# Optimization experiments

Hardware: AMD Instinct MI355X
Metric: run time of the kernel (lower is better)

## Reference

```python
import jax, jax.numpy as jnp
import numpy as np

V_WORD, V_CHAR = 50000, 128
EMB, CEMB, FILT, K = 300, 32, 4, 3
HID = 512
T, B, W = 128, 64, 16
OUT = 20
CCH = CEMB * FILT  # 128 conv output channels
LSTM_IN = EMB + CCH  # 428


def setup_inputs() -> dict:
    key = jax.random.key(0)
    ks = jax.random.split(key, 20)
    s = 0.1  # matches init_weights std
    inp = {
        "words": jax.random.randint(ks[0], (T, B), 0, V_WORD),
        "chars": jax.random.randint(ks[1], (B, T, W), 0, V_CHAR),
        "emb_W": s * jax.random.normal(ks[2], (V_WORD, EMB), jnp.float32),
        "char_emb_W": s * jax.random.normal(ks[3], (V_CHAR, CEMB), jnp.float32),
        "conv_W": s * jax.random.normal(ks[4], (CCH, 1, K), jnp.float32),
        "conv_b": s * jax.random.normal(ks[5], (CCH,), jnp.float32),
        "Wih_f": s * jax.random.normal(ks[6], (4 * HID, LSTM_IN), jnp.float32),
        "Whh_f": s * jax.random.normal(ks[7], (4 * HID, HID), jnp.float32),
        "bih_f": s * jax.random.normal(ks[8], (4 * HID,), jnp.float32),
        "bhh_f": s * jax.random.normal(ks[9], (4 * HID,), jnp.float32),
        "Wih_b": s * jax.random.normal(ks[10], (4 * HID, LSTM_IN), jnp.float32),
        "Whh_b": s * jax.random.normal(ks[11], (4 * HID, HID), jnp.float32),
        "bih_b": s * jax.random.normal(ks[12], (4 * HID,), jnp.float32),
        "bhh_b": s * jax.random.normal(ks[13], (4 * HID,), jnp.float32),
        "fc_W": s * jax.random.normal(ks[14], (OUT, 2 * HID), jnp.float32),
        "fc_b": s * jax.random.normal(ks[15], (OUT,), jnp.float32),
    }
    return inp


def _lstm_dir(x, Wih, Whh, bih, bhh):
    # x: [T, B, I] -> hs: [T, B, H]; PyTorch gate order i, f, g, o
    H = Whh.shape[1]
    b = bih + bhh
    xW = jnp.einsum("tbi,gi->tbg", x, Wih) + b  # precompute input projections

    def step(carry, xt):
        h, c = carry
        z = xt + h @ Whh.T  # [B, 4H]
        i, f, g, o = jnp.split(z, 4, axis=-1)
        c = jax.nn.sigmoid(f) * c + jax.nn.sigmoid(i) * jnp.tanh(g)
        h = jax.nn.sigmoid(o) * jnp.tanh(c)
        return (h, c), h

    h0 = jnp.zeros((x.shape[1], H), x.dtype)
    _, hs = jax.lax.scan(step, (h0, h0), xW)
    return hs


def reference(words, chars, emb_W, char_emb_W, conv_W, conv_b,
              Wih_f, Whh_f, bih_f, bhh_f, Wih_b, Whh_b, bih_b, bhh_b,
              fc_W, fc_b):
    # word embeddings: [T, B, EMB]
    emb_out = emb_W[words]
    # char embeddings: [B, T, W, CEMB] -> batched depthwise-grouped conv over all words at once
    ce = char_emb_W[chars]
    x = ce.reshape(B * T, W, CEMB).transpose(0, 2, 1)  # [B*T, CEMB, W]
    conv = jax.lax.conv_general_dilated(
        x, conv_W, window_strides=(1,), padding="VALID",
        feature_group_count=CEMB,
        dimension_numbers=("NCH", "OIH", "NCH"))  # [B*T, CCH, W-K+1]
    conv = conv + conv_b[None, :, None]
    char_cnn_max = conv.max(axis=2).reshape(B, T, CCH)  # [B, T, CCH]
    char_cnn_p = char_cnn_max.transpose(1, 0, 2)  # [T, B, CCH]
    feat = jnp.concatenate([emb_out, char_cnn_p], axis=2)  # [T, B, 428]
    h_f = _lstm_dir(feat, Wih_f, Whh_f, bih_f, bhh_f)
    h_b = _lstm_dir(feat[::-1], Wih_b, Whh_b, bih_b, bhh_b)[::-1]
    lstm_out = jnp.concatenate([h_f, h_b], axis=2)  # [T, B, 2H]
    return lstm_out @ fc_W.T + fc_b  # [T, B, OUT]
```

## Files before the change

kernel.cpp:

```cpp
#include <hip/hip_runtime.h>
#include <hip/hip_bf16.h>

#define TT 128
#define BATCH 64
#define WCH 16
#define CEMB 32
#define CCH 128
#define HID 512
#define GATES 2048
#define INF_ 428
#define KP 448
#define NOUT 20

typedef float f32x4 __attribute__((ext_vector_type(4)));
typedef __bf16 b8v __attribute__((ext_vector_type(8)));
typedef unsigned int u32x2 __attribute__((ext_vector_type(2)));
typedef unsigned int u32x4 __attribute__((ext_vector_type(4)));
typedef __hip_bfloat16 bf16;

__device__ __forceinline__ float sigm(float x){ return 1.f/(1.f+__expf(-x)); }
__device__ __forceinline__ float tanh_(float x){ float e=__expf(2.f*x); return (e-1.f)/(e+1.f); }

__global__ __launch_bounds__(256) void k_prep(
    const int* __restrict__ words, const int* __restrict__ chars,
    const float* __restrict__ embW, const float* __restrict__ cembW,
    const float* __restrict__ convW, const float* __restrict__ convb,
    const float* __restrict__ WihF, const float* __restrict__ WhhF,
    const float* __restrict__ bihF, const float* __restrict__ bhhF,
    const float* __restrict__ WihB, const float* __restrict__ WhhB,
    const float* __restrict__ bihB, const float* __restrict__ bhhB,
    bf16* __restrict__ featb, bf16* __restrict__ Wihp,
    bf16* __restrict__ Whhp, float* __restrict__ bsum) {
  const int tid = threadIdx.x;
  if (blockIdx.x < 4096) {
    int r = blockIdx.x*2 + (tid >> 7);
    int t2 = tid & 127;
    int t = r >> 6, b = r & 63;
    int wi = words[t*BATCH + b];
    const float* src = embW + (size_t)wi * 300;
    bf16* dst = featb + (size_t)r * KP;
    for (int k = t2; k < 300; k += 128) dst[k] = __float2bfloat16(src[k]);
    if (t2 < KP - INF_) dst[INF_ + t2] = __float2bfloat16(0.f);
    int cc = t2, g = cc >> 2;
    const int* ch = chars + ((size_t)b*TT + t)*WCH;
    float ce[WCH];
    #pragma unroll
    for (int w = 0; w < WCH; ++w) ce[w] = cembW[ch[w]*CEMB + g];
    float w0 = convW[cc*3], w1 = convW[cc*3+1], w2 = convW[cc*3+2];
    float m = -1e30f;
    #pragma unroll
    for (int p = 0; p < WCH-2; ++p) m = fmaxf(m, ce[p]*w0 + ce[p+1]*w1 + ce[p+2]*w2);
    dst[300 + cc] = __float2bfloat16(m + convb[cc]);
  } else {
    size_t tid0 = (size_t)(blockIdx.x - 4096)*256 + tid;
    size_t nthr = (size_t)2048*256;
    for (size_t idx = tid0; idx < (size_t)2*GATES*HID; idx += nthr) {
      int k = idx & (HID-1);
      int p = (idx >> 9) & (GATES-1);
      int d = (int)(idx >> 20);
      int j = ((p>>5)<<3) | (p&7);
      int tau = (p>>3)&3;
      const float* Whh = d ? WhhB : WhhF;
      Whhp[idx] = __float2bfloat16(Whh[(size_t)(tau*HID + j)*HID + k]);
    }
    for (size_t idx = tid0; idx < (size_t)2*GATES*KP; idx += nthr) {
      int k = (int)(idx % KP);
      size_t rest = idx / KP;
      int p = (int)(rest & (GATES-1));
      int d = (int)(rest >> 11);
      int j = ((p>>5)<<3) | (p&7);
      int tau = (p>>3)&3;
      const float* Wih = d ? WihB : WihF;
      float v = (k < INF_) ? Wih[(size_t)(tau*HID + j)*INF_ + k] : 0.f;
      Wihp[idx] = __float2bfloat16(v);
    }
    for (size_t idx = tid0; idx < (size_t)2*GATES; idx += nthr) {
      int p = (int)(idx & (GATES-1));
      int d = (int)(idx >> 11);
      int j = ((p>>5)<<3) | (p&7);
      int tau = (p>>3)&3;
      int gg = tau*HID + j;
      bsum[idx] = d ? (bihB[gg]+bhhB[gg]) : (bihF[gg]+bhhF[gg]);
    }
  }
}

__global__ __launch_bounds__(256) void k_gemm(const bf16* __restrict__ Wihp,
      const bf16* __restrict__ featb, const float* __restrict__ bsum,
      bf16* __restrict__ xW) {
  __shared__ short As[128][72];
  __shared__ short Bs[128][72];
  int m0 = (blockIdx.x & 31) << 7;
  int n0 = (blockIdx.x >> 5) << 7;
  int tid = threadIdx.x;
  int lane = tid & 63;
  int wid = tid >> 6;
  int wr = wid >> 1, wc = wid & 1;
  int lm = lane & 15, kg = lane >> 4;
  f32x4 acc[4][4] = {};
  for (int k0 = 0; k0 < KP; k0 += 64) {
    #pragma unroll
    for (int c = 0; c < 4; ++c) {
      int ch = tid + c*256;
      int row = ch >> 3, k8 = (ch & 7) << 3;
      *(b8v*)&As[row][k8] = *(const b8v*)&Wihp[(size_t)(m0+row)*KP + k0 + k8];
      *(b8v*)&Bs[row][k8] = *(const b8v*)&featb[(size_t)(n0+row)*KP + k0 + k8];
    }
    __syncthreads();
    #pragma unroll
    for (int ks = 0; ks < 2; ++ks) {
      b8v a[4], bb[4];
      #pragma unroll
      for (int i = 0; i < 4; ++i) a[i]  = *(const b8v*)&As[wr*64 + i*16 + lm][ks*32 + kg*8];
      #pragma unroll
      for (int i = 0; i < 4; ++i) bb[i] = *(const b8v*)&Bs[wc*64 + i*16 + lm][ks*32 + kg*8];
      #pragma unroll
      for (int mi = 0; mi < 4; ++mi)
        #pragma unroll
        for (int ni = 0; ni < 4; ++ni)
          acc[mi][ni] = __builtin_amdgcn_mfma_f32_16x16x32_bf16(a[mi], bb[ni], acc[mi][ni], 0, 0, 0);
    }
    __syncthreads();
  }
  #pragma unroll
  for (int mi = 0; mi < 4; ++mi) {
    #pragma unroll
    for (int ni = 0; ni < 4; ++ni) {
      int r = n0 + wc*64 + ni*16 + lm;
      int t = r >> 6, b = r & 63;
      #pragma unroll
      for (int reg = 0; reg < 4; ++reg) {
        int G = m0 + wr*64 + mi*16 + kg*4 + reg;
        int d = G >> 11, p = G & (GATES-1);
        int jt_ = p >> 5, pp = p & 31;
        int noff = ((pp>>2)&3)*8 + (pp>>4)*4 + (pp&3);
        float v = acc[mi][ni][reg] + bsum[G];
        xW[(((size_t)t*2 + d)*64 + jt_)*2048 + b*32 + noff] = __float2bfloat16(v);
      }
    }
  }
}

__global__ __launch_bounds__(256, 1) void k_persist(
    const bf16* __restrict__ Whhp, const bf16* __restrict__ xW,
    bf16* __restrict__ hs, unsigned* __restrict__ flags) {
  __shared__ __align__(16) bf16 hlds[16*512];
  const int tid = threadIdx.x;
  const int widx = tid >> 6;
  const int wid = blockIdx.x*4 + widx;
  const int lane = tid & 63;
  const int dir = wid >> 8;
  const int btile = (wid >> 6) & 3;
  const int jt = wid & 63;
  const int grp = blockIdx.x >> 4;
  const int wv = ((blockIdx.x & 15) << 2) | widx;
  const int b0 = btile << 4, pbase = jt << 5, jbase = jt << 3;
  const int col = lane & 15, kg = lane >> 4;

  u32x4 wq0[16], wq1[16];
  {
    const bf16* wp = Whhp + (size_t)dir*GATES*HID;
    #pragma unroll
    for (int ks = 0; ks < 16; ++ks) {
      wq0[ks] = *(const u32x4*)&wp[(size_t)(pbase + col)*HID + ks*32 + kg*8];
      wq1[ks] = *(const u32x4*)&wp[(size_t)(pbase + 16 + col)*HID + ks*32 + kg*8];
    }
    #pragma unroll
    for (int ks = 0; ks < 16; ++ks) {
      asm volatile("" : "+v"(wq0[ks]));
      asm volatile("" : "+v"(wq1[ks]));
    }
  }
  const bf16* const xwbase = xW + (size_t)jt*2048 + (b0 + col)*32 + kg*8;
  b8v nx;
  {
    const int t0 = dir ? TT-1 : 0;
    nx = *(const b8v*)(xwbase + (size_t)(t0*2 + dir)*64*2048);
  }
  f32x4 creg = {0.f, 0.f, 0.f, 0.f};

  for (int step = 0; step < TT; ++step) {
    const int tcur = dir ? (TT-1-step) : step;
    f32x4 acc0, acc1;
    if (step > 0) {
      if (widx == 0) {
        const unsigned* fp = flags + (((size_t)(step-1)*8 + grp) << 6) + lane;
        for (;;) {
          unsigned v;
          asm volatile("global_load_dword %0, %1, off sc0 sc1\n\ts_waitcnt vmcnt(0)"
                       : "=v"(v) : "v"(fp) : "memory");
          if (__all(v == (unsigned)step)) break;
        }
      }
      __syncthreads();
      const int tprev = dir ? tcur+1 : tcur-1;
      const bf16* hbase = hs + (((size_t)dir*TT + tprev)*BATCH + b0)*HID;
      u32x4 tmp0, tmp1, tmp2, tmp3;
      {
        const bf16* a0 = hbase + (size_t)tid*8;
        const bf16* a1 = a0 + 2048;
        const bf16* a2 = a0 + 4096;
        const bf16* a3 = a0 + 6144;
        asm volatile("global_load_dwordx4 %0, %1, off sc0 sc1" : "=v"(tmp0) : "v"(a0) : "memory");
        asm volatile("global_load_dwordx4 %0, %1, off sc0 sc1" : "=v"(tmp1) : "v"(a1) : "memory");
        asm volatile("global_load_dwordx4 %0, %1, off sc0 sc1" : "=v"(tmp2) : "v"(a2) : "memory");
        asm volatile("global_load_dwordx4 %0, %1, off sc0 sc1" : "=v"(tmp3) : "v"(a3) : "memory");
      }
      asm volatile("s_waitcnt vmcnt(0)" ::: "memory");
      __builtin_amdgcn_sched_barrier(0);
      #pragma unroll
      for (int p = 0; p < 4; ++p) {
        int c = p*256 + tid;
        int b = c >> 6, j8 = c & 63;
        int slot = j8 ^ (b & 7);
        u32x4 val = (p==0) ? tmp0 : (p==1) ? tmp1 : (p==2) ? tmp2 : tmp3;
        *(u32x4*)&hlds[b*512 + slot*8] = val;
      }
      __syncthreads();
      #pragma unroll
      for (int r = 0; r < 4; ++r) { acc0[r] = (float)nx[r]; acc1[r] = (float)nx[r+4]; }
      #pragma unroll
      for (int ks = 0; ks < 16; ++ks) {
        int slotr = (ks*4 + kg) ^ (col & 7);
        b8v bfrag = *(const b8v*)&hlds[col*512 + slotr*8];
        acc0 = __builtin_amdgcn_mfma_f32_16x16x32_bf16(__builtin_bit_cast(b8v, wq0[ks]), bfrag, acc0, 0, 0, 0);
        acc1 = __builtin_amdgcn_mfma_f32_16x16x32_bf16(__builtin_bit_cast(b8v, wq1[ks]), bfrag, acc1, 0, 0, 0);
      }
    } else {
      #pragma unroll
      for (int r = 0; r < 4; ++r) { acc0[r] = (float)nx[r]; acc1[r] = (float)nx[r+4]; }
    }
    f32x4 fsh, osh;
    #pragma unroll
    for (int r = 0; r < 4; ++r) {
      fsh[r] = __shfl_xor(acc0[r], 32);
      osh[r] = __shfl_xor(acc1[r], 32);
    }
    if (lane < 32) {
      unsigned us[4];
      #pragma unroll
      for (int r = 0; r < 4; ++r) {
        float zi = acc0[r], zf = fsh[r], zg = acc1[r], zo = osh[r];
        float co = (step > 0) ? creg[r] : 0.f;
        float cn = sigm(zf)*co + sigm(zi)*tanh_(zg);
        creg[r] = cn;
        us[r] = (unsigned)__builtin_bit_cast(unsigned short, __float2bfloat16(sigm(zo)*tanh_(cn)));
      }
      u32x2 pk; pk.x = us[0] | (us[1] << 16); pk.y = us[2] | (us[3] << 16);
      bf16* hpw = hs + (((size_t)dir*TT + tcur)*BATCH + b0 + col)*HID + jbase + kg*4;
      asm volatile("global_store_dwordx2 %0, %1, off sc0 sc1"
                   :: "v"(hpw), "v"(pk) : "memory");
    }
    if (step + 1 < TT) {
      asm volatile("s_waitcnt vmcnt(0)" ::: "memory");
      if (lane == 0) {
        unsigned* fw = flags + (((size_t)step*8 + grp) << 6) + wv;
        unsigned val = (unsigned)(step + 1);
        asm volatile("global_store_dword %0, %1, off sc0 sc1"
                     :: "v"(fw), "v"(val) : "memory");
      }
      const int tnext = dir ? tcur-1 : tcur+1;
      nx = *(const b8v*)(xwbase + (size_t)(tnext*2 + dir)*64*2048);
    }
  }
}

__global__ __launch_bounds__(256) void k_fc(const bf16* __restrict__ hs,
                     const float* __restrict__ fcW,
                     const float* __restrict__ fcb, float* __restrict__ out) {
  int t = blockIdx.x;
  for (int item = threadIdx.x; item < BATCH*NOUT; item += 256) {
    const int b = item / NOUT, o = item - b*NOUT;
    const b8v* hf8 = (const b8v*)(hs + ((size_t)t*BATCH + b)*HID);
    const b8v* hb8 = (const b8v*)(hs + (((size_t)TT + t)*BATCH + b)*HID);
    const float4* w4 = (const float4*)(fcW + (size_t)o*2*HID);
    float s = fcb[o];
    #pragma unroll 4
    for (int k = 0; k < 64; ++k) {
      b8v hv = hf8[k];
      float4 wa = w4[2*k], wb = w4[2*k+1];
      s += (float)hv[0]*wa.x + (float)hv[1]*wa.y + (float)hv[2]*wa.z + (float)hv[3]*wa.w
         + (float)hv[4]*wb.x + (float)hv[5]*wb.y + (float)hv[6]*wb.z + (float)hv[7]*wb.w;
    }
    #pragma unroll 4
    for (int k = 0; k < 64; ++k) {
      b8v hv = hb8[k];
      float4 wa = w4[128 + 2*k], wb = w4[129 + 2*k];
      s += (float)hv[0]*wa.x + (float)hv[1]*wa.y + (float)hv[2]*wa.z + (float)hv[3]*wa.w
         + (float)hv[4]*wb.x + (float)hv[5]*wb.y + (float)hv[6]*wb.z + (float)hv[7]*wb.w;
    }
    out[((size_t)t*BATCH + b)*NOUT + o] = s;
  }
}

extern "C" void kernel_launch(void* const* d_in, const int* in_sizes, int n_in,
                              void* d_out, int out_size, void* d_ws, size_t ws_size,
                              hipStream_t stream) {
  const int* words = (const int*)d_in[0];
  const int* chars = (const int*)d_in[1];
  const float* embW = (const float*)d_in[2];
  const float* cembW = (const float*)d_in[3];
  const float* convW = (const float*)d_in[4];
  const float* convb = (const float*)d_in[5];
  const float* WihF = (const float*)d_in[6];
  const float* WhhF = (const float*)d_in[7];
  const float* bihF = (const float*)d_in[8];
  const float* bhhF = (const float*)d_in[9];
  const float* WihB = (const float*)d_in[10];
  const float* WhhB = (const float*)d_in[11];
  const float* bihB = (const float*)d_in[12];
  const float* bhhB = (const float*)d_in[13];
  const float* fcW = (const float*)d_in[14];
  const float* fcb = (const float*)d_in[15];
  float* out = (float*)d_out;

  char* ws = (char*)d_ws;
  size_t off = 0;
  bf16* xW    = (bf16*)(ws + off); off += (size_t)TT*2*GATES*BATCH*2;
  bf16* hsbuf = (bf16*)(ws + off); off += (size_t)2*TT*BATCH*HID*2;
  bf16* featb = (bf16*)(ws + off); off += (size_t)TT*BATCH*KP*2;
  bf16* Wihp  = (bf16*)(ws + off); off += (size_t)2*GATES*KP*2;
  bf16* Whhp  = (bf16*)(ws + off); off += (size_t)2*GATES*HID*2;
  float* bsum = (float*)(ws + off); off += (size_t)2*GATES*4;
  unsigned* flags = (unsigned*)(ws + off); off += (size_t)TT*8*64*4;
  if (off > ws_size) return;

  hipMemsetAsync(flags, 0, (size_t)TT*8*64*4, stream);
  k_prep<<<6144, 256, 0, stream>>>(words, chars, embW, cembW, convW, convb,
                                   WihF, WhhF, bihF, bhhF, WihB, WhhB, bihB, bhhB,
                                   featb, Wihp, Whhp, bsum);
  k_gemm<<<2048, 256, 0, stream>>>(Wihp, featb, bsum, xW);
  k_persist<<<128, 256, 0, stream>>>(Whhp, xW, hsbuf, flags);
  k_fc<<<TT, 256, 0, stream>>>(hsbuf, fcW, fcb, out);
}
```

Measured before the change: 654.0 us.

## Fuse input-projection GEMM into persistent LSTM kernel with per-timestep readiness flags

Merges the input-projection GEMM and the persistent recurrent kernel into one launch. Blocks 0-127 run the recurrence while blocks 128-255 compute GEMM tiles, ordered so the timesteps needed first by the forward and backward directions (from both ends of the sequence) finish early. Each GEMM tile bumps a per-timestep-pair counter, and recurrent waves spin on it before loading the next xW slice. This overlaps the GEMM with the serial recurrence instead of running it as a separate upfront phase. It also vectorises the xW epilogue stores, but relies on all 256 blocks being co-resident and adds polling overhead on the recurrence's critical path.

```diff
diff --git a/kernel.cpp b/kernel.cpp
--- a/kernel.cpp
+++ b/kernel.cpp
@@ -85,67 +85,82 @@
   }
 }
 
-__global__ __launch_bounds__(256) void k_gemm(const bf16* __restrict__ Wihp,
-      const bf16* __restrict__ featb, const float* __restrict__ bsum,
-      bf16* __restrict__ xW) {
-  __shared__ short As[128][72];
-  __shared__ short Bs[128][72];
-  int m0 = (blockIdx.x & 31) << 7;
-  int n0 = (blockIdx.x >> 5) << 7;
-  int tid = threadIdx.x;
-  int lane = tid & 63;
-  int wid = tid >> 6;
-  int wr = wid >> 1, wc = wid & 1;
-  int lm = lane & 15, kg = lane >> 4;
-  f32x4 acc[4][4] = {};
-  for (int k0 = 0; k0 < KP; k0 += 64) {
-    #pragma unroll
-    for (int c = 0; c < 4; ++c) {
-      int ch = tid + c*256;
-      int row = ch >> 3, k8 = (ch & 7) << 3;
-      *(b8v*)&As[row][k8] = *(const b8v*)&Wihp[(size_t)(m0+row)*KP + k0 + k8];
-      *(b8v*)&Bs[row][k8] = *(const b8v*)&featb[(size_t)(n0+row)*KP + k0 + k8];
-    }
-    __syncthreads();
-    #pragma unroll
-    for (int ks = 0; ks < 2; ++ks) {
-      b8v a[4], bb[4];
-      #pragma unroll
-      for (int i = 0; i < 4; ++i) a[i]  = *(const b8v*)&As[wr*64 + i*16 + lm][ks*32 + kg*8];
-      #pragma unroll
-      for (int i = 0; i < 4; ++i) bb[i] = *(const b8v*)&Bs[wc*64 + i*16 + lm][ks*32 + kg*8];
-      #pragma unroll
-      for (int mi = 0; mi < 4; ++mi)
+__global__ __launch_bounds__(256, 1) void k_fused(
+    const bf16* __restrict__ Whhp, const bf16* __restrict__ Wihp,
+    const bf16* __restrict__ featb, const float* __restrict__ bsum,
+    bf16* __restrict__ xW, bf16* __restrict__ hs,
+    unsigned* __restrict__ flags, unsigned* __restrict__ tflags) {
+  __shared__ __align__(16) char smem[36864];
+  const int tid = threadIdx.x;
+
+  if (blockIdx.x >= 128) {
+    typedef short sh72[72];
+    sh72* As = (sh72*)smem;
+    sh72* Bs = (sh72*)(smem + 18432);
+    const int g = blockIdx.x - 128;
+    const int lane = tid & 63;
+    const int wid4 = tid >> 6;
+    const int wr = wid4 >> 1, wc = wid4 & 1;
+    const int lm = lane & 15, kg = lane >> 4;
+    for (int q = g; q < 2048; q += 128) {
+      const int n_ord = q >> 5, m = q & 31;
+      const int nblk = (n_ord & 1) ? (63 - (n_ord >> 1)) : (n_ord >> 1);
+      const int m0 = m << 7, n0 = nblk << 7;
+      f32x4 acc[4][4] = {};
+      for (int k0 = 0; k0 < KP; k0 += 64) {
         #pragma unroll
-        for (int ni = 0; ni < 4; ++ni)
-          acc[mi][ni] = __builtin_amdgcn_mfma_f32_16x16x32_bf16(a[mi], bb[ni], acc[mi][ni], 0, 0, 0);
-    }
-    __syncthreads();
-  }
-  #pragma unroll
-  for (int mi = 0; mi < 4; ++mi) {
-    #pragma unroll
-    for (int ni = 0; ni < 4; ++ni) {
-      int r = n0 + wc*64 + ni*16 + lm;
-      int t = r >> 6, b = r & 63;
-      #pragma unroll
-      for (int reg = 0; reg < 4; ++reg) {
-        int G = m0 + wr*64 + mi*16 + kg*4 + reg;
-        int d = G >> 11, p = G & (GATES-1);
-        int jt_ = p >> 5, pp = p & 31;
-        int noff = ((pp>>2)&3)*8 + (pp>>4)*4 + (pp&3);
-        float v = acc[mi][ni][reg] + bsum[G];
-        xW[(((size_t)t*2 + d)*64 + jt_)*2048 + b*32 + noff] = __float2bfloat16(v);
-      }
-    }
-  }
-}
-
-__global__ __launch_bounds__(256, 1) void k_persist(
-    const bf16* __restrict__ Whhp, const bf16* __restrict__ xW,
-    bf16* __restrict__ hs, unsigned* __restrict__ flags) {
-  __shared__ __align__(16) bf16 hlds[16*512];
-  const int tid = threadIdx.x;
+        for (int c = 0; c < 4; ++c) {
+          int ch = tid + c*256;
+          int row = ch >> 3, k8 = (ch & 7) << 3;
+          *(b8v*)&As[row][k8] = *(const b8v*)&Wihp[(size_t)(m0+row)*KP + k0 + k8];
+          *(b8v*)&Bs[row][k8] = *(const b8v*)&featb[(size_t)(n0+row)*KP + k0 + k8];
+        }
+        __syncthreads();
+        #pragma unroll
+        for (int ks = 0; ks < 2; ++ks) {
+          b8v a[4], bb[4];
+          #pragma unroll
+          for (int i = 0; i < 4; ++i) a[i]  = *(const b8v*)&As[wr*64 + i*16 + lm][ks*32 + kg*8];
+          #pragma unroll
+          for (int i = 0; i < 4; ++i) bb[i] = *(const b8v*)&Bs[wc*64 + i*16 + lm][ks*32 + kg*8];
+          #pragma unroll
+          for (int mi = 0; mi < 4; ++mi)
+            #pragma unroll
+            for (int ni = 0; ni < 4; ++ni)
+              acc[mi][ni] = __builtin_amdgcn_mfma_f32_16x16x32_bf16(a[mi], bb[ni], acc[mi][ni], 0, 0, 0);
+        }
+        __syncthreads();
+      }
+      #pragma unroll
+      for (int mi = 0; mi < 4; ++mi) {
+        #pragma unroll
+        for (int ni = 0; ni < 4; ++ni) {
+          int r = n0 + wc*64 + ni*16 + lm;
+          int t = r >> 6, b = r & 63;
+          int G = m0 + wr*64 + mi*16 + kg*4;
+          int d = G >> 11, p = G & (GATES-1);
+          int jt_ = p >> 5, pp = p & 31;
+          int noff = ((pp>>2)&3)*8 + (pp>>4)*4;
+          unsigned us[4];
+          #pragma unroll
+          for (int reg = 0; reg < 4; ++reg) {
+            float v = acc[mi][ni][reg] + bsum[G + reg];
+            us[reg] = (unsigned)__builtin_bit_cast(unsigned short, __float2bfloat16(v));
+          }
+          u32x2 pk; pk.x = us[0] | (us[1] << 16); pk.y = us[2] | (us[3] << 16);
+          bf16* dst = xW + (((size_t)t*2 + d)*64 + jt_)*2048 + b*32 + noff;
+          asm volatile("global_store_dwordx2 %0, %1, off sc0 sc1"
+                       :: "v"(dst), "v"(pk) : "memory");
+        }
+      }
+      asm volatile("s_waitcnt vmcnt(0)" ::: "memory");
+      __syncthreads();
+      if (tid == 0) atomicAdd(&tflags[nblk], 1u);
+    }
+    return;
+  }
+
+  bf16* hlds = (bf16*)smem;
   const int widx = tid >> 6;
   const int wid = blockIdx.x*4 + widx;
   const int lane = tid & 63;
@@ -172,10 +187,19 @@
     }
   }
   const bf16* const xwbase = xW + (size_t)jt*2048 + (b0 + col)*32 + kg*8;
-  b8v nx;
+  u32x4 nxu;
   {
     const int t0 = dir ? TT-1 : 0;
-    nx = *(const b8v*)(xwbase + (size_t)(t0*2 + dir)*64*2048);
+    const unsigned* tf0 = tflags + (t0 >> 1);
+    unsigned tv;
+    do {
+      asm volatile("global_load_dword %0, %1, off sc0 sc1\n\ts_waitcnt vmcnt(0)"
+                   : "=v"(tv) : "v"(tf0) : "memory");
+    } while (tv < 32u);
+    const bf16* xaddr = xwbase + (size_t)(t0*2 + dir)*64*2048;
+    asm volatile("global_load_dwordx4 %0, %1, off sc0 sc1\n\ts_waitcnt vmcnt(0)"
+                 : "=v"(nxu) : "v"(xaddr) : "memory");
+    __builtin_amdgcn_sched_barrier(0);
   }
   f32x4 creg = {0.f, 0.f, 0.f, 0.f};
 
@@ -217,6 +241,7 @@
         *(u32x4*)&hlds[b*512 + slot*8] = val;
       }
       __syncthreads();
+      b8v nx = __builtin_bit_cast(b8v, nxu);
       #pragma unroll
       for (int r = 0; r < 4; ++r) { acc0[r] = (float)nx[r]; acc1[r] = (float)nx[r+4]; }
       #pragma unroll
@@ -227,6 +252,7 @@
         acc1 = __builtin_amdgcn_mfma_f32_16x16x32_bf16(__builtin_bit_cast(b8v, wq1[ks]), bfrag, acc1, 0, 0, 0);
       }
     } else {
+      b8v nx = __builtin_bit_cast(b8v, nxu);
       #pragma unroll
       for (int r = 0; r < 4; ++r) { acc0[r] = (float)nx[r]; acc1[r] = (float)nx[r+4]; }
     }
@@ -252,6 +278,10 @@
                    :: "v"(hpw), "v"(pk) : "memory");
     }
     if (step + 1 < TT) {
+      const int tnext = dir ? tcur-1 : tcur+1;
+      const unsigned* tf = tflags + (tnext >> 1);
+      unsigned tv;
+      asm volatile("global_load_dword %0, %1, off sc0 sc1" : "=v"(tv) : "v"(tf) : "memory");
       asm volatile("s_waitcnt vmcnt(0)" ::: "memory");
       if (lane == 0) {
         unsigned* fw = flags + (((size_t)step*8 + grp) << 6) + wv;
@@ -259,8 +289,13 @@
         asm volatile("global_store_dword %0, %1, off sc0 sc1"
                      :: "v"(fw), "v"(val) : "memory");
       }
-      const int tnext = dir ? tcur-1 : tcur+1;
-      nx = *(const b8v*)(xwbase + (size_t)(tnext*2 + dir)*64*2048);
+      while (tv < 32u) {
+        asm volatile("global_load_dword %0, %1, off sc0 sc1\n\ts_waitcnt vmcnt(0)"
+                     : "=v"(tv) : "v"(tf) : "memory");
+      }
+      const bf16* xaddr = xwbase + (size_t)(tnext*2 + dir)*64*2048;
+      asm volatile("global_load_dwordx4 %0, %1, off sc0 sc1"
+                   : "=v"(nxu) : "v"(xaddr) : "memory");
     }
   }
 }
@@ -323,13 +358,13 @@
   bf16* Whhp  = (bf16*)(ws + off); off += (size_t)2*GATES*HID*2;
   float* bsum = (float*)(ws + off); off += (size_t)2*GATES*4;
   unsigned* flags = (unsigned*)(ws + off); off += (size_t)TT*8*64*4;
+  unsigned* tflags = (unsigned*)(ws + off); off += 4096;
   if (off > ws_size) return;
 
-  hipMemsetAsync(flags, 0, (size_t)TT*8*64*4, stream);
+  hipMemsetAsync(flags, 0, (size_t)TT*8*64*4 + 4096, stream);
   k_prep<<<6144, 256, 0, stream>>>(words, chars, embW, cembW, convW, convb,
                                    WihF, WhhF, bihF, bhhF, WihB, WhhB, bihB, bhhB,
                                    featb, Wihp, Whhp, bsum);
-  k_gemm<<<2048, 256, 0, stream>>>(Wihp, featb, bsum, xW);
-  k_persist<<<128, 256, 0, stream>>>(Whhp, xW, hsbuf, flags);
+  k_fused<<<256, 256, 0, stream>>>(Whhp, Wihp, featb, bsum, xW, hsbuf, flags, tflags);
   k_fc<<<TT, 256, 0, stream>>>(hsbuf, fcW, fcb, out);
 }
```

After: 699.7 us. 7.0% more time.
